# Optimization experiments

Hardware: AMD Instinct MI355X
Metric: run time of the kernel (lower is better)

The kernel has to match this reference:

```python
import jax, jax.numpy as jnp
import numpy as np

N, D = 2048, 64


def setup_inputs() -> dict:
    key = jax.random.key(0)
    x = jax.random.normal(key, (N, D), dtype=jnp.float32)
    return {"x": x}


def reference(x):
    # torch scan over rows i: rd_i = sqrt(sum((x - x_i)^2, axis=1))
    # Stacked result is the full self-cdist matrix [N, N].
    diff = x[:, None, :] - x[None, :, :]        # [N, N, D] (row i = samex - x_i)
    sq_sum = jnp.sum(diff * diff, axis=-1)      # [N, N]
    return jnp.sqrt(sq_sum)
```

## Files before the change

### kernel.cpp

```cpp
#include <hip/hip_runtime.h>
#include <math.h>

#define NN 2048
#define DD 64
#define BT 64
#define LDK (128 + 8)

typedef short short8 __attribute__((ext_vector_type(8)));
typedef float f32x4 __attribute__((ext_vector_type(4)));
typedef unsigned short us4 __attribute__((ext_vector_type(4)));

__device__ inline unsigned short f2bf(float f) {
    unsigned u = __float_as_uint(f);
    return (unsigned short)((u + 0x7FFFu + ((u >> 16) & 1u)) >> 16);
}
__device__ inline float bf2f(unsigned short b) {
    return __uint_as_float(((unsigned)b) << 16);
}

__global__ __launch_bounds__(256, 4) void cdist_mfma(const float* __restrict__ x,
                                                     float* __restrict__ out) {
    __shared__ unsigned short CA[BT][LDK];
    __shared__ unsigned short CB[BT][LDK];
    __shared__ float nrmA[BT], nrmB[BT];

    const int tid = threadIdx.x;
    const int bi = blockIdx.y * BT;
    const int bj = blockIdx.x * BT;

    #pragma unroll
    for (int p = 0; p < 2; ++p) {
        const float4* src = (const float4*)(x + (size_t)(p ? bj : bi) * DD);
        unsigned short (*C)[LDK] = p ? CB : CA;
        #pragma unroll
        for (int s = 0; s < 4; ++s) {
            int idx = tid + s * 256;
            int row = idx >> 4;
            int c4  = (idx & 15) << 2;
            float4 v = src[idx];
            unsigned short h0 = f2bf(v.x), h1 = f2bf(v.y), h2 = f2bf(v.z), h3 = f2bf(v.w);
            us4 hv = {h0, h1, h2, h3};
            us4 lv = {f2bf(v.x - bf2f(h0)), f2bf(v.y - bf2f(h1)),
                      f2bf(v.z - bf2f(h2)), f2bf(v.w - bf2f(h3))};
            *(us4*)(&C[row][c4])      = hv;
            *(us4*)(&C[row][64 + c4]) = lv;
        }
    }

    if (tid < 128) {
        int r = tid & 63;
        const float4* row = (const float4*)(x + (size_t)((tid < 64 ? bi : bj) + r) * DD);
        float s = 0.f;
        #pragma unroll
        for (int q = 0; q < 16; ++q) {
            float4 v = row[q];
            s = fmaf(v.x, v.x, s); s = fmaf(v.y, v.y, s);
            s = fmaf(v.z, v.z, s); s = fmaf(v.w, v.w, s);
        }
        if (tid < 64) nrmA[r] = s; else nrmB[r] = s;
    }
    __syncthreads();

    const int lane = tid & 63;
    const int wid  = tid >> 6;
    const int wm = wid >> 1, wn = wid & 1;
    const int lr = lane & 15;
    const int lk = (lane >> 4) * 8;

    f32x4 acc[2][2] = {};
    #pragma unroll
    for (int ks = 0; ks < 4; ++ks) {
        const int k = ks * 32 + lk;
        short8 af[2], bfr[2];
        #pragma unroll
        for (int m = 0; m < 2; ++m)
            af[m] = *(const short8*)(&CA[wm * 32 + m * 16 + lr][k]);
        #pragma unroll
        for (int n = 0; n < 2; ++n)
            bfr[n] = *(const short8*)(&CB[wn * 32 + n * 16 + lr][k]);
        #pragma unroll
        for (int m = 0; m < 2; ++m)
            #pragma unroll
            for (int n = 0; n < 2; ++n)
                acc[m][n] = __builtin_amdgcn_mfma_f32_16x16x32_bf16(af[m], bfr[n], acc[m][n], 0, 0, 0);
    }

    #pragma unroll
    for (int m = 0; m < 2; ++m) {
        #pragma unroll
        for (int g = 0; g < 4; ++g) {
            const int row = wm * 32 + m * 16 + (lane >> 4) * 4 + g;
            const float na = nrmA[row];
            const int gi = bi + row;
            float* orow = out + (size_t)gi * NN + bj;
            #pragma unroll
            for (int n = 0; n < 2; ++n) {
                const int col = wn * 32 + n * 16 + lr;
                const int gj = bj + col;
                float v = na + nrmB[col] - 2.f * acc[m][n][g];
                float d = sqrtf(fmaxf(v, 0.f));
                orow[col] = (gi == gj) ? 0.f : d;
            }
        }
    }
}

extern "C" void kernel_launch(void* const* d_in, const int* in_sizes, int n_in,
                              void* d_out, int out_size, void* d_ws, size_t ws_size,
                              hipStream_t stream) {
    const float* x = (const float*)d_in[0];
    float* out = (float*)d_out;
    dim3 grid(NN / BT, NN / BT);
    cdist_mfma<<<grid, dim3(256), 0, stream>>>(x, out);
}
```

Measured before the change: 14.95 us.

## Precompute bf16 hi/lo split and norms in prep kernel, drop LDS staging

```diff
diff --git a/kernel.cpp b/kernel.cpp
--- a/kernel.cpp
+++ b/kernel.cpp
@@ -4,7 +4,7 @@
 #define NN 2048
 #define DD 64
 #define BT 64
-#define LDK (128 + 8)
+#define CK 128
 
 typedef short short8 __attribute__((ext_vector_type(8)));
 typedef float f32x4 __attribute__((ext_vector_type(4)));
@@ -18,89 +18,76 @@
     return __uint_as_float(((unsigned)b) << 16);
 }
 
-__global__ __launch_bounds__(256, 4) void cdist_mfma(const float* __restrict__ x,
-                                                     float* __restrict__ out) {
-    __shared__ unsigned short CA[BT][LDK];
-    __shared__ unsigned short CB[BT][LDK];
-    __shared__ float nrmA[BT], nrmB[BT];
+__global__ __launch_bounds__(256) void prep(const float* __restrict__ x,
+                                            unsigned short* __restrict__ C,
+                                            float* __restrict__ nrm) {
+    const int idx = blockIdx.x * 256 + threadIdx.x;
+    const int row = idx >> 4;
+    const int c4  = (idx & 15) << 2;
+    float4 v = ((const float4*)x)[idx];
+    unsigned short h0 = f2bf(v.x), h1 = f2bf(v.y), h2 = f2bf(v.z), h3 = f2bf(v.w);
+    us4 hv = {h0, h1, h2, h3};
+    us4 lv = {f2bf(v.x - bf2f(h0)), f2bf(v.y - bf2f(h1)),
+              f2bf(v.z - bf2f(h2)), f2bf(v.w - bf2f(h3))};
+    *(us4*)(C + (size_t)row * CK + c4)      = hv;
+    *(us4*)(C + (size_t)row * CK + 64 + c4) = lv;
+    float s = 0.f;
+    s = fmaf(v.x, v.x, s); s = fmaf(v.y, v.y, s);
+    s = fmaf(v.z, v.z, s); s = fmaf(v.w, v.w, s);
+    s += __shfl_xor(s, 1, 16);
+    s += __shfl_xor(s, 2, 16);
+    s += __shfl_xor(s, 4, 16);
+    s += __shfl_xor(s, 8, 16);
+    if ((idx & 15) == 0) nrm[row] = s;
+}
 
-    const int tid = threadIdx.x;
-    const int bi = blockIdx.y * BT;
-    const int bj = blockIdx.x * BT;
-
-    #pragma unroll
-    for (int p = 0; p < 2; ++p) {
-        const float4* src = (const float4*)(x + (size_t)(p ? bj : bi) * DD);
-        unsigned short (*C)[LDK] = p ? CB : CA;
-        #pragma unroll
-        for (int s = 0; s < 4; ++s) {
-            int idx = tid + s * 256;
-            int row = idx >> 4;
-            int c4  = (idx & 15) << 2;
-            float4 v = src[idx];
-            unsigned short h0 = f2bf(v.x), h1 = f2bf(v.y), h2 = f2bf(v.z), h3 = f2bf(v.w);
-            us4 hv = {h0, h1, h2, h3};
-            us4 lv = {f2bf(v.x - bf2f(h0)), f2bf(v.y - bf2f(h1)),
-                      f2bf(v.z - bf2f(h2)), f2bf(v.w - bf2f(h3))};
-            *(us4*)(&C[row][c4])      = hv;
-            *(us4*)(&C[row][64 + c4]) = lv;
-        }
-    }
-
-    if (tid < 128) {
-        int r = tid & 63;
-        const float4* row = (const float4*)(x + (size_t)((tid < 64 ? bi : bj) + r) * DD);
-        float s = 0.f;
-        #pragma unroll
-        for (int q = 0; q < 16; ++q) {
-            float4 v = row[q];
-            s = fmaf(v.x, v.x, s); s = fmaf(v.y, v.y, s);
-            s = fmaf(v.z, v.z, s); s = fmaf(v.w, v.w, s);
-        }
-        if (tid < 64) nrmA[r] = s; else nrmB[r] = s;
-    }
-    __syncthreads();
-
+__global__ __launch_bounds__(256, 6) void cdist_g(const unsigned short* __restrict__ C,
+                                                  const float* __restrict__ nrm,
+                                                  float* __restrict__ out) {
+    const int tid  = threadIdx.x;
+    const int bi   = blockIdx.y * BT;
+    const int bj   = blockIdx.x * BT;
     const int lane = tid & 63;
     const int wid  = tid >> 6;
     const int wm = wid >> 1, wn = wid & 1;
     const int lr = lane & 15;
     const int lk = (lane >> 4) * 8;
 
+    const short8* A0 = (const short8*)(C + (size_t)(bi + wm * 32 + lr) * CK + lk);
+    const short8* A1 = (const short8*)(C + (size_t)(bi + wm * 32 + 16 + lr) * CK + lk);
+    const short8* B0 = (const short8*)(C + (size_t)(bj + wn * 32 + lr) * CK + lk);
+    const short8* B1 = (const short8*)(C + (size_t)(bj + wn * 32 + 16 + lr) * CK + lk);
+
     f32x4 acc[2][2] = {};
     #pragma unroll
     for (int ks = 0; ks < 4; ++ks) {
-        const int k = ks * 32 + lk;
-        short8 af[2], bfr[2];
-        #pragma unroll
-        for (int m = 0; m < 2; ++m)
-            af[m] = *(const short8*)(&CA[wm * 32 + m * 16 + lr][k]);
-        #pragma unroll
-        for (int n = 0; n < 2; ++n)
-            bfr[n] = *(const short8*)(&CB[wn * 32 + n * 16 + lr][k]);
-        #pragma unroll
-        for (int m = 0; m < 2; ++m)
-            #pragma unroll
-            for (int n = 0; n < 2; ++n)
-                acc[m][n] = __builtin_amdgcn_mfma_f32_16x16x32_bf16(af[m], bfr[n], acc[m][n], 0, 0, 0);
+        short8 a0 = A0[ks * 4];
+        short8 a1 = A1[ks * 4];
+        short8 b0 = B0[ks * 4];
+        short8 b1 = B1[ks * 4];
+        acc[0][0] = __builtin_amdgcn_mfma_f32_16x16x32_bf16(a0, b0, acc[0][0], 0, 0, 0);
+        acc[0][1] = __builtin_amdgcn_mfma_f32_16x16x32_bf16(a0, b1, acc[0][1], 0, 0, 0);
+        acc[1][0] = __builtin_amdgcn_mfma_f32_16x16x32_bf16(a1, b0, acc[1][0], 0, 0, 0);
+        acc[1][1] = __builtin_amdgcn_mfma_f32_16x16x32_bf16(a1, b1, acc[1][1], 0, 0, 0);
     }
+
+    const float nb0 = nrm[bj + wn * 32 + lr];
+    const float nb1 = nrm[bj + wn * 32 + 16 + lr];
 
     #pragma unroll
     for (int m = 0; m < 2; ++m) {
         #pragma unroll
         for (int g = 0; g < 4; ++g) {
             const int row = wm * 32 + m * 16 + (lane >> 4) * 4 + g;
-            const float na = nrmA[row];
-            const int gi = bi + row;
+            const int gi  = bi + row;
+            const float na = nrm[gi];
             float* orow = out + (size_t)gi * NN + bj;
-            #pragma unroll
-            for (int n = 0; n < 2; ++n) {
-                const int col = wn * 32 + n * 16 + lr;
-                const int gj = bj + col;
-                float v = na + nrmB[col] - 2.f * acc[m][n][g];
-                float d = sqrtf(fmaxf(v, 0.f));
-                orow[col] = (gi == gj) ? 0.f : d;
-            }
+            const int col0 = wn * 32 + lr;
+            float v0 = na + nb0 - 2.f * acc[m][0][g];
+            orow[col0] = (gi == bj + col0) ? 0.f : sqrtf(fmaxf(v0, 0.f));
+            const int col1 = wn * 32 + 16 + lr;
+            float v1 = na + nb1 - 2.f * acc[m][1][g];
+            orow[col1] = (gi == bj + col1) ? 0.f : sqrtf(fmaxf(v1, 0.f));
         }
     }
 }
@@ -110,6 +97,8 @@
                               hipStream_t stream) {
     const float* x = (const float*)d_in[0];
     float* out = (float*)d_out;
-    dim3 grid(NN / BT, NN / BT);
-    cdist_mfma<<<grid, dim3(256), 0, stream>>>(x, out);
+    unsigned short* C = (unsigned short*)d_ws;
+    float* nrm = (float*)((char*)d_ws + (size_t)NN * CK * 2);
+    prep<<<dim3(128), dim3(256), 0, stream>>>(x, C, nrm);
+    cdist_g<<<dim3(NN / BT, NN / BT), dim3(256), 0, stream>>>(C, nrm, out);
 }
```

Result: slower. 22.95 us (+53.5%).
